# Optimization experiments

Hardware: AMD Instinct MI355X
Metric: run time of the kernel (lower is better)

The kernel has to match this reference:

```python
import jax, jax.numpy as jnp
import numpy as np

DIM = 1024
N_HEADS = 16
HEAD_DIM = DIM // N_HEADS


def setup_inputs() -> dict:
    key = jax.random.key(0)
    ks = jax.random.split(key, 7)
    B, S = 2, 2048
    scale = 0.02
    return {
        "q": jax.random.normal(ks[0], (B, S, DIM), dtype=jnp.float32),
        "k": jax.random.normal(ks[1], (B, S, DIM), dtype=jnp.float32),
        "v": jax.random.normal(ks[2], (B, S, DIM), dtype=jnp.float32),
        # torch nn.Linear weights are [out_features, in_features]; y = x @ W.T
        "wq": jax.random.normal(ks[3], (DIM, DIM), dtype=jnp.float32) * scale,
        "wk": jax.random.normal(ks[4], (DIM, DIM), dtype=jnp.float32) * scale,
        "wv": jax.random.normal(ks[5], (DIM, DIM), dtype=jnp.float32) * scale,
        "wo": jax.random.normal(ks[6], (DIM, DIM), dtype=jnp.float32) * scale,
    }


def reference(q, k, v, wq, wk, wv, wo):
    B, S, _ = q.shape
    H, D = N_HEADS, HEAD_DIM
    # projections (torch Linear: x @ W.T), reshape to [B, H, S, D]
    xq = (q @ wq.T).reshape(B, S, H, D).transpose(0, 2, 1, 3)
    xk = (k @ wk.T).reshape(B, S, H, D).transpose(0, 2, 1, 3)
    xv = (v @ wv.T).reshape(B, S, H, D).transpose(0, 2, 1, 3)
    # scaled dot-product attention with causal mask
    scores = jnp.einsum("bhqd,bhkd->bhqk", xq, xk) / jnp.sqrt(jnp.float32(D))
    causal = jnp.tril(jnp.ones((S, S), dtype=bool))
    scores = jnp.where(causal, scores, -jnp.inf)
    attn = jax.nn.softmax(scores.astype(jnp.float32), axis=-1).astype(xq.dtype)
    # dropout prob = 0.0 (eval-mode / deterministic reference)
    out = jnp.einsum("bhqk,bhkd->bhqd", attn, xv)
    out = out.transpose(0, 2, 1, 3).reshape(B, S, H * D)
    return out @ wo.T
```

## Files before the change

kernel.cpp:

```cpp
#include <hip/hip_runtime.h>
#include <hip/hip_bf16.h>
#include <stdint.h>


typedef short s16x8 __attribute__((ext_vector_type(8)));
typedef float f32x4 __attribute__((ext_vector_type(4)));

#define MFMA_BF16 __builtin_amdgcn_mfma_f32_16x16x32_bf16

static __device__ __forceinline__ unsigned short f2bf(float f) {
    union { float f; unsigned u; } x{f};
    unsigned r = x.u + 0x7fff + ((x.u >> 16) & 1);
    return (unsigned short)(r >> 16);
}
static __device__ __forceinline__ unsigned pk2h(float a, float b) {
    __hip_bfloat162 h = __float22bfloat162_rn(float2{a, b});
    return *(unsigned*)&h;
}
static __device__ __forceinline__ void ald16(unsigned short* lds, const unsigned short* g) {
    __builtin_amdgcn_global_load_lds(
        (const __attribute__((address_space(1))) unsigned int*)g,
        (__attribute__((address_space(3))) unsigned int*)lds, 16, 0, 0);
}

#define QSCL 0.18033688f

__global__ __launch_bounds__(256) void convert_all_kernel(
        const float* __restrict__ q, const float* __restrict__ k,
        const float* __restrict__ v,
        const float* __restrict__ wq, const float* __restrict__ wk,
        const float* __restrict__ wv, const float* __restrict__ wo,
        unsigned short* __restrict__ dst) {
    const size_t idx = ((size_t)blockIdx.x * 256 + threadIdx.x) * 8;
    const int region = (int)(idx >> 22);
    const float* src;
    size_t off;
    if (region == 0)      { src = q; off = idx; }
    else if (region == 1) { src = k; off = idx & 4194303; }
    else if (region == 2) { src = v; off = idx & 4194303; }
    else {
        const int wsel = (int)((idx >> 20) & 3);
        src = wsel == 0 ? wq : wsel == 1 ? wk : wsel == 2 ? wv : wo;
        off = idx & 1048575;
    }
    const float4* p = (const float4*)(src + off);
    float4 a = p[0], b = p[1];
    uint4 u;
    u.x = pk2h(a.x, a.y); u.y = pk2h(a.z, a.w);
    u.z = pk2h(b.x, b.y); u.w = pk2h(b.z, b.w);
    *(uint4*)(dst + idx) = u;
}

__global__ __launch_bounds__(256) void proj3b_kernel(
        const unsigned short* __restrict__ Qb, const unsigned short* __restrict__ Kb,
        const unsigned short* __restrict__ Vb, const unsigned short* __restrict__ Wb,
        unsigned short* __restrict__ Xq, unsigned short* __restrict__ Xk,
        unsigned short* __restrict__ Xvt) {
    constexpr int Kd = 1024;
    __shared__ union {
        struct { unsigned short A[128 * 32]; unsigned short B[128 * 32]; } s;
        unsigned short T[4 * 64 * 68];
    } sm;

    const int z = blockIdx.z;
    const unsigned short* A  = z == 0 ? Qb : z == 1 ? Kb : Vb;
    const unsigned short* Bw = Wb + (size_t)z * 1048576;

    const int t = threadIdx.x;
    const int m0 = blockIdx.x * 128, n0 = blockIdx.y * 128;
    const int w = t >> 6, lane = t & 63, fr = lane & 15, g = lane >> 4;
    const int wm = (w >> 1) * 64, wn = (w & 1) * 64;
    const int brow = t >> 2;
    const int cB = (t & 3) ^ ((t >> 3) & 3);
    const int sB = g ^ ((fr >> 1) & 3);

    f32x4 acc[4][4] = {};

    for (int k0 = 0; k0 < Kd; k0 += 32) {
        ald16(sm.s.A + (size_t)w * 512,        A  + (size_t)(m0 + brow) * Kd + k0 + cB * 8);
        ald16(sm.s.A + 2048 + (size_t)w * 512, A  + (size_t)(m0 + 64 + brow) * Kd + k0 + cB * 8);
        ald16(sm.s.B + (size_t)w * 512,        Bw + (size_t)(n0 + brow) * Kd + k0 + cB * 8);
        ald16(sm.s.B + 2048 + (size_t)w * 512, Bw + (size_t)(n0 + 64 + brow) * Kd + k0 + cB * 8);
        __syncthreads();

        s16x8 af[4], bfv[4];
#pragma unroll
        for (int mi = 0; mi < 4; ++mi)
            af[mi] = *(const s16x8*)(sm.s.A + (wm + mi * 16 + fr) * 32 + sB * 8);
#pragma unroll
        for (int ni = 0; ni < 4; ++ni)
            bfv[ni] = *(const s16x8*)(sm.s.B + (wn + ni * 16 + fr) * 32 + sB * 8);
#pragma unroll
        for (int mi = 0; mi < 4; ++mi)
#pragma unroll
            for (int ni = 0; ni < 4; ++ni)
                acc[mi][ni] = MFMA_BF16(af[mi], bfv[ni], acc[mi][ni], 0, 0, 0);
        __syncthreads();
    }

    if (z != 2) {
        unsigned short* C = z ? Xk : Xq;
        const float osc = z == 0 ? QSCL : 1.0f;
#pragma unroll
        for (int mi = 0; mi < 4; ++mi)
#pragma unroll
            for (int ni = 0; ni < 4; ++ni)
#pragma unroll
                for (int reg = 0; reg < 4; ++reg)
                    C[(size_t)(m0 + wm + mi * 16 + g * 4 + reg) * 1024 +
                      n0 + wn + ni * 16 + fr] = f2bf(acc[mi][ni][reg] * osc);
    } else {
        unsigned short* T = sm.T + w * (64 * 68);
#pragma unroll
        for (int mi = 0; mi < 4; ++mi)
#pragma unroll
            for (int ni = 0; ni < 4; ++ni) {
                uint2 u;
                u.x = pk2h(acc[mi][ni][0], acc[mi][ni][1]);
                u.y = pk2h(acc[mi][ni][2], acc[mi][ni][3]);
                *(uint2*)(T + (ni * 16 + fr) * 68 + mi * 16 + g * 4) = u;
            }
        __asm__ __volatile__("" ::: "memory");
#pragma unroll
        for (int pass = 0; pass < 8; ++pass) {
            const int row = pass * 8 + (lane >> 3);
            const int chk = lane & 7;
            uint4 d = *(const uint4*)(T + row * 68 + chk * 8);
            *(uint4*)(Xvt + (size_t)(n0 + wn + row) * 4096 + m0 + wm + chk * 8) = d;
        }
    }
}

__global__ __launch_bounds__(256, 4) void flash_attn_kernel(
        const unsigned short* __restrict__ Xq, const unsigned short* __restrict__ Xk,
        const unsigned short* __restrict__ Xvt, unsigned short* __restrict__ Oa) {
    __shared__ unsigned short Kls[64 * 64];
    __shared__ unsigned short Vls[64 * 64];
    __shared__ unsigned short Pls[4][16 * 64];

    const int t = threadIdx.x;
    const int bh = blockIdx.x;
    const int qt = blockIdx.y;
    const int b = bh >> 4, h = bh & 15;
    const size_t rbase = (size_t)b * 2048;
    const int cbase = h * 64;

    const int w = t >> 6, lane = t & 63, fr = lane & 15, g = lane >> 4, fq = g * 8;
    const int qrow = qt * 64 + w * 16 + fr;

    const unsigned short* qp = Xq + (rbase + qrow) * 1024 + cbase;
    s16x8 qf0 = *(const s16x8*)(qp + fq);
    s16x8 qf1 = *(const s16x8*)(qp + 32 + fq);

    float l_i = 0.f;
    f32x4 oacc[4] = {};

    const int r0 = w * 16 + (lane >> 3), r1 = r0 + 8;
    const int s8 = lane & 7;
    const int c0 = s8 ^ (r0 & 7), c1 = s8 ^ (r1 & 7);
    const unsigned short* kbase = Xk + rbase * 1024 + cbase;
    const size_t vrow0 = (size_t)(cbase + r0) * 4096 + rbase + c0 * 8;
    const size_t vrow1 = (size_t)(cbase + r1) * 4096 + rbase + c1 * 8;

    uint4 kA, kB, vA, vB;
    kA = *(const uint4*)(kbase + (size_t)r0 * 1024 + c0 * 8);
    kB = *(const uint4*)(kbase + (size_t)r1 * 1024 + c1 * 8);
    vA = *(const uint4*)(Xvt + vrow0);
    vB = *(const uint4*)(Xvt + vrow1);

    for (int kt = 0; kt <= qt; ++kt) {
        *(uint4*)(Kls + (w * 16) * 64 + lane * 8)     = kA;
        *(uint4*)(Kls + (w * 16 + 8) * 64 + lane * 8) = kB;
        *(uint4*)(Vls + (w * 16) * 64 + lane * 8)     = vA;
        *(uint4*)(Vls + (w * 16 + 8) * 64 + lane * 8) = vB;
        __syncthreads();

        if (kt < qt) {
            const unsigned short* ks = kbase + (size_t)(kt + 1) * 65536;
            kA = *(const uint4*)(ks + (size_t)r0 * 1024 + c0 * 8);
            kB = *(const uint4*)(ks + (size_t)r1 * 1024 + c1 * 8);
            vA = *(const uint4*)(Xvt + vrow0 + (size_t)(kt + 1) * 64);
            vB = *(const uint4*)(Xvt + vrow1 + (size_t)(kt + 1) * 64);
        }

        f32x4 sf[4];
#pragma unroll
        for (int m16 = 0; m16 < 4; ++m16) {
            const int rr = m16 * 16 + fr;
            s16x8 kf0 = *(const s16x8*)(Kls + rr * 64 + ((g ^ (fr & 7)) * 8));
            s16x8 kf1 = *(const s16x8*)(Kls + rr * 64 + (((4 + g) ^ (fr & 7)) * 8));
            f32x4 zz = {};
            zz = MFMA_BF16(kf0, qf0, zz, 0, 0, 0);
            sf[m16] = MFMA_BF16(kf1, qf1, zz, 0, 0, 0);
        }

        float e[4][4];
        const bool diag = (kt == qt);
#pragma unroll
        for (int m16 = 0; m16 < 4; ++m16)
#pragma unroll
            for (int r = 0; r < 4; ++r) {
                float x = sf[m16][r];
                if (diag) {
                    const int keyg = kt * 64 + m16 * 16 + g * 4 + r;
                    x = (keyg <= qrow) ? x : -1e30f;
                }
                const float ee = exp2f(x);
                e[m16][r] = ee;
                l_i += ee;
            }

        unsigned short* Pw = &Pls[w][0];
#pragma unroll
        for (int m16 = 0; m16 < 4; ++m16) {
            uint2 u;
            u.x = pk2h(e[m16][0], e[m16][1]);
            u.y = pk2h(e[m16][2], e[m16][3]);
            const int ch = 2 * m16 + (g >> 1);
            *(uint2*)(Pw + fr * 64 + ((ch ^ (fr & 7)) * 8) + (g & 1) * 4) = u;
        }
        __asm__ __volatile__("" ::: "memory");
        s16x8 pf0 = *(const s16x8*)(Pw + fr * 64 + ((g ^ (fr & 7)) * 8));
        s16x8 pf1 = *(const s16x8*)(Pw + fr * 64 + (((4 + g) ^ (fr & 7)) * 8));

#pragma unroll
        for (int m16 = 0; m16 < 4; ++m16) {
            const int rr = m16 * 16 + fr;
            s16x8 vf0 = *(const s16x8*)(Vls + rr * 64 + ((g ^ (fr & 7)) * 8));
            s16x8 vf1 = *(const s16x8*)(Vls + rr * 64 + (((4 + g) ^ (fr & 7)) * 8));
            oacc[m16] = MFMA_BF16(vf0, pf0, oacc[m16], 0, 0, 0);
            oacc[m16] = MFMA_BF16(vf1, pf1, oacc[m16], 0, 0, 0);
        }
        __syncthreads();
    }

    l_i += __shfl_xor(l_i, 16, 64);
    l_i += __shfl_xor(l_i, 32, 64);
    const float inv = 1.0f / l_i;
#pragma unroll
    for (int m16 = 0; m16 < 4; ++m16) {
        uint2 u;
        u.x = pk2h(oacc[m16][0] * inv, oacc[m16][1] * inv);
        u.y = pk2h(oacc[m16][2] * inv, oacc[m16][3] * inv);
        *(uint2*)(Oa + (rbase + qrow) * 1024 + cbase + m16 * 16 + g * 4) = u;
    }
}

__global__ __launch_bounds__(256) void outproj_kernel(
        const unsigned short* __restrict__ Oa, const unsigned short* __restrict__ Wo,
        float* __restrict__ out) {
    constexpr int Kd = 1024;
    __shared__ unsigned short lsA[64 * 32];
    __shared__ unsigned short lsB[128 * 32];

    const int t = threadIdx.x;
    const int m0 = blockIdx.x * 64, n0 = blockIdx.y * 128;
    const int w = t >> 6, lane = t & 63, fr = lane & 15, g = lane >> 4;
    const int wm = (w >> 1) * 32, wn = (w & 1) * 64;
    const int brow = t >> 2;
    const int cB = (t & 3) ^ ((t >> 3) & 3);
    const int sB = g ^ ((fr >> 1) & 3);

    f32x4 acc[2][4] = {};

    for (int k0 = 0; k0 < Kd; k0 += 32) {
        ald16(lsA + (size_t)w * 512,        Oa + (size_t)(m0 + brow) * Kd + k0 + cB * 8);
        ald16(lsB + (size_t)w * 512,        Wo + (size_t)(n0 + brow) * Kd + k0 + cB * 8);
        ald16(lsB + 2048 + (size_t)w * 512, Wo + (size_t)(n0 + 64 + brow) * Kd + k0 + cB * 8);
        __syncthreads();

        s16x8 af[2], bfv[4];
#pragma unroll
        for (int mi = 0; mi < 2; ++mi)
            af[mi] = *(const s16x8*)(lsA + (wm + mi * 16 + fr) * 32 + sB * 8);
#pragma unroll
        for (int ni = 0; ni < 4; ++ni)
            bfv[ni] = *(const s16x8*)(lsB + (wn + ni * 16 + fr) * 32 + sB * 8);
#pragma unroll
        for (int mi = 0; mi < 2; ++mi)
#pragma unroll
            for (int ni = 0; ni < 4; ++ni)
                acc[mi][ni] = MFMA_BF16(af[mi], bfv[ni], acc[mi][ni], 0, 0, 0);
        __syncthreads();
    }

#pragma unroll
    for (int mi = 0; mi < 2; ++mi)
#pragma unroll
        for (int ni = 0; ni < 4; ++ni)
#pragma unroll
            for (int reg = 0; reg < 4; ++reg)
                out[(size_t)(m0 + wm + mi * 16 + g * 4 + reg) * 1024 +
                    n0 + wn + ni * 16 + fr] = acc[mi][ni][reg];
}

extern "C" void kernel_launch(void* const* d_in, const int* in_sizes, int n_in,
                              void* d_out, int out_size, void* d_ws, size_t ws_size,
                              hipStream_t stream) {
    const float* q  = (const float*)d_in[0];
    const float* k  = (const float*)d_in[1];
    const float* v  = (const float*)d_in[2];
    const float* wq = (const float*)d_in[3];
    const float* wk = (const float*)d_in[4];
    const float* wv = (const float*)d_in[5];
    const float* wo = (const float*)d_in[6];
    float* out = (float*)d_out;

    unsigned short* base = (unsigned short*)d_ws;
    unsigned short* Qb  = base;
    unsigned short* Kb  = base + 4194304;
    unsigned short* Vb  = base + 8388608;
    unsigned short* Wb  = base + 12582912;
    unsigned short* Xq  = base + 16777216;
    unsigned short* Xk  = base + 20971520;
    unsigned short* Xvt = base + 25165824;
    unsigned short* Oa  = base + 29360128;

    convert_all_kernel<<<8192, 256, 0, stream>>>(q, k, v, wq, wk, wv, wo, base);
    proj3b_kernel<<<dim3(32, 8, 3), 256, 0, stream>>>(Qb, Kb, Vb, Wb, Xq, Xk, Xvt);
    flash_attn_kernel<<<dim3(32, 32), 256, 0, stream>>>(Xq, Xk, Xvt, Oa);
    outproj_kernel<<<dim3(64, 8), 256, 0, stream>>>(Oa, Wb + 3145728, out);
}
```

Measured before the change: 217.3 us.

## Split attention work across warps by key subtile and reduce partial outputs in LDS

Each warp now takes one 16-key slice of each 64-key tile against all four 16-row query groups, instead of one query group against all keys. Each warp keeps the probabilities in registers as half-zero MFMA operands, which drops the per-warp LDS round trip for P. Warps skip fully masked diagonal subtiles, and query tiles are launched in reverse order so the long causal rows start first. The price is 4x larger output accumulators (lower occupancy, launch bounds 3), half-wasted MFMA K-width, and a final cross-warp tree reduction of partial O and row sums through LDS.

Result: no change. 218.2 us (+0.4%).

```diff
diff --git a/kernel.cpp b/kernel.cpp
--- a/kernel.cpp
+++ b/kernel.cpp
@@ -131,42 +131,52 @@
     }
 }
 
-__global__ __launch_bounds__(256, 4) void flash_attn_kernel(
+__global__ __launch_bounds__(256, 3) void flash_attn_kernel(
         const unsigned short* __restrict__ Xq, const unsigned short* __restrict__ Xk,
         const unsigned short* __restrict__ Xvt, unsigned short* __restrict__ Oa) {
-    __shared__ unsigned short Kls[64 * 64];
-    __shared__ unsigned short Vls[64 * 64];
-    __shared__ unsigned short Pls[4][16 * 64];
+    __shared__ union {
+        struct { unsigned short K[64 * 64]; unsigned short V[64 * 64]; } s;
+        struct { float o[2][16][64][4]; float l[2][64][4]; } r;
+    } sm;
 
     const int t = threadIdx.x;
     const int bh = blockIdx.x;
-    const int qt = blockIdx.y;
+    const int qt = 31 - (int)blockIdx.y;
     const int b = bh >> 4, h = bh & 15;
     const size_t rbase = (size_t)b * 2048;
     const int cbase = h * 64;
 
-    const int w = t >> 6, lane = t & 63, fr = lane & 15, g = lane >> 4, fq = g * 8;
-    const int qrow = qt * 64 + w * 16 + fr;
-
-    const unsigned short* qp = Xq + (rbase + qrow) * 1024 + cbase;
-    s16x8 qf0 = *(const s16x8*)(qp + fq);
-    s16x8 qf1 = *(const s16x8*)(qp + 32 + fq);
-
-    float l_i = 0.f;
-    f32x4 oacc[4] = {};
+    const int w = t >> 6, lane = t & 63, fr = lane & 15, g = lane >> 4;
+
+    s16x8 qf[4][2];
+#pragma unroll
+    for (int qg = 0; qg < 4; ++qg) {
+        const unsigned short* qp = Xq + (rbase + qt * 64 + qg * 16 + fr) * 1024 + cbase;
+        qf[qg][0] = *(const s16x8*)(qp + g * 8);
+        qf[qg][1] = *(const s16x8*)(qp + 32 + g * 8);
+    }
+
+    float lacc[4] = {0.f, 0.f, 0.f, 0.f};
+    f32x4 oacc[4][4] = {};
 
     const int r0 = w * 16 + (lane >> 3), r1 = r0 + 8;
-    const int s8 = lane & 7;
-    const int c0 = s8 ^ (r0 & 7), c1 = s8 ^ (r1 & 7);
+    const int s8l = lane & 7;
+    const int c0 = s8l ^ (r0 & 7), c1 = s8l ^ (r1 & 7);
     const unsigned short* kbase = Xk + rbase * 1024 + cbase;
     const size_t vrow0 = (size_t)(cbase + r0) * 4096 + rbase + c0 * 8;
     const size_t vrow1 = (size_t)(cbase + r1) * 4096 + rbase + c1 * 8;
 
-    uint4 kA, kB, vA, vB;
-    kA = *(const uint4*)(kbase + (size_t)r0 * 1024 + c0 * 8);
-    kB = *(const uint4*)(kbase + (size_t)r1 * 1024 + c1 * 8);
-    vA = *(const uint4*)(Xvt + vrow0);
-    vB = *(const uint4*)(Xvt + vrow1);
+    uint4 kA = *(const uint4*)(kbase + (size_t)r0 * 1024 + c0 * 8);
+    uint4 kB = *(const uint4*)(kbase + (size_t)r1 * 1024 + c1 * 8);
+    uint4 vA = *(const uint4*)(Xvt + vrow0);
+    uint4 vB = *(const uint4*)(Xvt + vrow1);
+
+    unsigned short* Kls = sm.s.K;
+    unsigned short* Vls = sm.s.V;
+    const int rowK = w * 16 + fr;
+    const int kslot0 = (g ^ (fr & 7)) * 8;
+    const int kslot1 = ((4 + g) ^ (fr & 7)) * 8;
+    const int vchunk = 2 * w + (g >> 1);
 
     for (int kt = 0; kt <= qt; ++kt) {
         *(uint4*)(Kls + (w * 16) * 64 + lane * 8)     = kA;
@@ -183,66 +193,85 @@
             vB = *(const uint4*)(Xvt + vrow1 + (size_t)(kt + 1) * 64);
         }
 
-        f32x4 sf[4];
-#pragma unroll
-        for (int m16 = 0; m16 < 4; ++m16) {
-            const int rr = m16 * 16 + fr;
-            s16x8 kf0 = *(const s16x8*)(Kls + rr * 64 + ((g ^ (fr & 7)) * 8));
-            s16x8 kf1 = *(const s16x8*)(Kls + rr * 64 + (((4 + g) ^ (fr & 7)) * 8));
+        s16x8 kf0 = *(const s16x8*)(Kls + rowK * 64 + kslot0);
+        s16x8 kf1 = *(const s16x8*)(Kls + rowK * 64 + kslot1);
+        uint4 vfp[4];
+#pragma unroll
+        for (int mt = 0; mt < 4; ++mt) {
+            uint2 d2 = *(const uint2*)(Vls + (mt * 16 + fr) * 64 +
+                                       ((vchunk ^ (fr & 7)) * 8) + (g & 1) * 4);
+            vfp[mt].x = d2.x; vfp[mt].y = d2.y; vfp[mt].z = 0u; vfp[mt].w = 0u;
+        }
+
+        const bool diag = (kt == qt);
+#pragma unroll
+        for (int qg = 0; qg < 4; ++qg) {
+            if (diag && w > qg) continue;
             f32x4 zz = {};
-            zz = MFMA_BF16(kf0, qf0, zz, 0, 0, 0);
-            sf[m16] = MFMA_BF16(kf1, qf1, zz, 0, 0, 0);
-        }
-
-        float e[4][4];
-        const bool diag = (kt == qt);
-#pragma unroll
-        for (int m16 = 0; m16 < 4; ++m16)
-#pragma unroll
-            for (int r = 0; r < 4; ++r) {
-                float x = sf[m16][r];
-                if (diag) {
-                    const int keyg = kt * 64 + m16 * 16 + g * 4 + r;
-                    x = (keyg <= qrow) ? x : -1e30f;
-                }
-                const float ee = exp2f(x);
-                e[m16][r] = ee;
-                l_i += ee;
+            zz = MFMA_BF16(kf0, qf[qg][0], zz, 0, 0, 0);
+            f32x4 sf = MFMA_BF16(kf1, qf[qg][1], zz, 0, 0, 0);
+            float e[4];
+            const bool edge = diag && (w == qg);
+#pragma unroll
+            for (int r = 0; r < 4; ++r)
+                e[r] = (!edge || (g * 4 + r <= fr)) ? exp2f(sf[r]) : 0.f;
+            lacc[qg] += e[0] + e[1] + e[2] + e[3];
+            uint4 pu;
+            pu.x = pk2h(e[0], e[1]); pu.y = pk2h(e[2], e[3]); pu.z = 0u; pu.w = 0u;
+            const s16x8 pf = *(const s16x8*)&pu;
+#pragma unroll
+            for (int mt = 0; mt < 4; ++mt)
+                oacc[mt][qg] = MFMA_BF16(*(const s16x8*)&vfp[mt], pf,
+                                         oacc[mt][qg], 0, 0, 0);
+        }
+        __syncthreads();
+    }
+
+    auto wrbuf = [&](int bi) {
+#pragma unroll
+        for (int mt = 0; mt < 4; ++mt)
+#pragma unroll
+            for (int qg = 0; qg < 4; ++qg)
+                *(f32x4*)&sm.r.o[bi][mt * 4 + qg][lane][0] = oacc[mt][qg];
+        f32x4 lv = {lacc[0], lacc[1], lacc[2], lacc[3]};
+        *(f32x4*)&sm.r.l[bi][lane][0] = lv;
+    };
+    auto rdbuf = [&](int bi) {
+#pragma unroll
+        for (int mt = 0; mt < 4; ++mt)
+#pragma unroll
+            for (int qg = 0; qg < 4; ++qg)
+                oacc[mt][qg] += *(const f32x4*)&sm.r.o[bi][mt * 4 + qg][lane][0];
+        f32x4 lv = *(const f32x4*)&sm.r.l[bi][lane][0];
+        lacc[0] += lv[0]; lacc[1] += lv[1]; lacc[2] += lv[2]; lacc[3] += lv[3];
+    };
+    if (w == 1) wrbuf(0);
+    if (w == 3) wrbuf(1);
+    __syncthreads();
+    if (w == 0) rdbuf(0);
+    if (w == 2) rdbuf(1);
+    __syncthreads();
+    if (w == 2) wrbuf(0);
+    __syncthreads();
+    if (w == 0) {
+        rdbuf(0);
+#pragma unroll
+        for (int qg = 0; qg < 4; ++qg) {
+            lacc[qg] += __shfl_xor(lacc[qg], 16, 64);
+            lacc[qg] += __shfl_xor(lacc[qg], 32, 64);
+        }
+#pragma unroll
+        for (int qg = 0; qg < 4; ++qg) {
+            const float inv = 1.0f / lacc[qg];
+            const size_t row = rbase + qt * 64 + qg * 16 + fr;
+#pragma unroll
+            for (int mt = 0; mt < 4; ++mt) {
+                uint2 u;
+                u.x = pk2h(oacc[mt][qg][0] * inv, oacc[mt][qg][1] * inv);
+                u.y = pk2h(oacc[mt][qg][2] * inv, oacc[mt][qg][3] * inv);
+                *(uint2*)(Oa + row * 1024 + cbase + mt * 16 + g * 4) = u;
             }
-
-        unsigned short* Pw = &Pls[w][0];
-#pragma unroll
-        for (int m16 = 0; m16 < 4; ++m16) {
-            uint2 u;
-            u.x = pk2h(e[m16][0], e[m16][1]);
-            u.y = pk2h(e[m16][2], e[m16][3]);
-            const int ch = 2 * m16 + (g >> 1);
-            *(uint2*)(Pw + fr * 64 + ((ch ^ (fr & 7)) * 8) + (g & 1) * 4) = u;
-        }
-        __asm__ __volatile__("" ::: "memory");
-        s16x8 pf0 = *(const s16x8*)(Pw + fr * 64 + ((g ^ (fr & 7)) * 8));
-        s16x8 pf1 = *(const s16x8*)(Pw + fr * 64 + (((4 + g) ^ (fr & 7)) * 8));
-
-#pragma unroll
-        for (int m16 = 0; m16 < 4; ++m16) {
-            const int rr = m16 * 16 + fr;
-            s16x8 vf0 = *(const s16x8*)(Vls + rr * 64 + ((g ^ (fr & 7)) * 8));
-            s16x8 vf1 = *(const s16x8*)(Vls + rr * 64 + (((4 + g) ^ (fr & 7)) * 8));
-            oacc[m16] = MFMA_BF16(vf0, pf0, oacc[m16], 0, 0, 0);
-            oacc[m16] = MFMA_BF16(vf1, pf1, oacc[m16], 0, 0, 0);
-        }
-        __syncthreads();
-    }
-
-    l_i += __shfl_xor(l_i, 16, 64);
-    l_i += __shfl_xor(l_i, 32, 64);
-    const float inv = 1.0f / l_i;
-#pragma unroll
-    for (int m16 = 0; m16 < 4; ++m16) {
-        uint2 u;
-        u.x = pk2h(oacc[m16][0] * inv, oacc[m16][1] * inv);
-        u.y = pk2h(oacc[m16][2] * inv, oacc[m16][3] * inv);
-        *(uint2*)(Oa + (rbase + qrow) * 1024 + cbase + m16 * 16 + g * 4) = u;
+        }
     }
 }
 
```
